# Performance work log

Hardware: AMD Instinct MI355X
Metric: run time of the kernel (lower is better)

The kernel has to match this reference:

```python
import jax, jax.numpy as jnp
import numpy as np

B, NA, F, K, L = 96, 48, 128, 64, 6
CUT = 5.0


def _forward(pos, f_in, emb, msg_w1, msg_b1, msg_w2, msg_b2, rbf_w, rbf_b,
             upd_U, upd_V, upd_w1, upd_b1, upd_w2, upd_b2,
             out_w1, out_b1, out_w2, out_b2, node_atom):
    p = pos.reshape(B, NA, 3)
    rij = p[:, :, None, :] - p[:, None, :, :]          # [B,n,n,3], pos_i - pos_j
    d2 = jnp.sum(rij * rij, -1)
    eye = jnp.eye(NA, dtype=bool)
    d = jnp.sqrt(jnp.where(eye, 1.0, d2))              # safe sqrt on diagonal
    mask = (~eye) & (d < CUT)                          # radius_graph, loop=False
    centers = jnp.linspace(0.0, CUT, K)
    gamma = 1.0 / ((CUT / K) ** 2 + 1e-9)
    rbf = jnp.exp(-gamma * (d[..., None] - centers) ** 2)   # [B,n,n,K]
    cutf = 0.5 * (jnp.cos(jnp.pi * d / CUT) + 1.0)          # cosine cutoff
    w_env = jnp.where(mask, cutf, 0.0)[..., None]
    dirv = rij / d[..., None]                               # unit directions
    s = emb[node_atom].reshape(B, NA, F)
    v = jnp.zeros((B, NA, 3, F), s.dtype)
    for l in range(L):
        # message block
        phi = jax.nn.silu(s @ msg_w1[l] + msg_b1[l]) @ msg_w2[l] + msg_b2[l]  # [B,n,3F]
        Wf = (rbf @ rbf_w[l] + rbf_b[l]) * w_env                              # [B,n,n,3F]
        x = phi[:, None, :, :] * Wf                                           # phi of sender j
        ds, dvv, dvs = jnp.split(x, 3, axis=-1)
        s = s + ds.sum(2)
        v = v + jnp.einsum('bijf,bjcf->bicf', dvv, v) \
              + jnp.einsum('bijf,bijc->bicf', dvs, dirv)
        # update block
        Uv = jnp.einsum('bncf,fg->bncg', v, upd_U[l])
        Vv = jnp.einsum('bncf,fg->bncg', v, upd_V[l])
        Vn = jnp.sqrt(jnp.sum(Vv * Vv, 2) + 1e-8)                             # [B,n,F]
        a = jax.nn.silu(jnp.concatenate([s, Vn], -1) @ upd_w1[l] + upd_b1[l]) @ upd_w2[l] + upd_b2[l]
        avv, asv, ass = jnp.split(a, 3, -1)
        v = v + avv[:, :, None, :] * Uv
        s = s + asv * jnp.sum(Uv * Vv, 2) + ass
    out = jax.nn.silu(s @ out_w1 + out_b1) @ out_w2 + out_b2                  # [B,n,1]
    return out.sum(1)                                                         # per-graph sum


def setup_inputs() -> dict:
    key = jax.random.key(0)
    ks = jax.random.split(key, 16)
    N = B * NA
    pos = jax.random.normal(ks[0], (N, 3), jnp.float32) * 2.0
    f_in = jnp.zeros((N, 1), jnp.float32)
    node_atom = jax.random.randint(ks[1], (N,), 1, 84)
    batch = jnp.arange(N) // NA
    g = lambda k, shp, fan: jax.random.normal(k, shp, jnp.float32) / np.sqrt(fan)
    return dict(
        f_in=f_in, pos=pos, batch=batch, node_atom=node_atom,
        emb=g(ks[2], (100, F), 1.0),
        msg_w1=g(ks[3], (L, F, F), F), msg_b1=jnp.zeros((L, F), jnp.float32),
        msg_w2=g(ks[4], (L, F, 3 * F), F), msg_b2=jnp.zeros((L, 3 * F), jnp.float32),
        rbf_w=g(ks[5], (L, K, 3 * F), K), rbf_b=jnp.zeros((L, 3 * F), jnp.float32),
        upd_U=g(ks[6], (L, F, F), F), upd_V=g(ks[7], (L, F, F), F),
        upd_w1=g(ks[8], (L, 2 * F, F), 2 * F), upd_b1=jnp.zeros((L, F), jnp.float32),
        upd_w2=g(ks[9], (L, F, 3 * F), F), upd_b2=jnp.zeros((L, 3 * F), jnp.float32),
        out_w1=g(ks[10], (F, F), F), out_b1=jnp.zeros((F,), jnp.float32),
        out_w2=g(ks[11], (F, 1), F), out_b2=jnp.zeros((1,), jnp.float32),
    )


def reference(f_in, pos, batch, node_atom, emb, msg_w1, msg_b1, msg_w2, msg_b2,
              rbf_w, rbf_b, upd_U, upd_V, upd_w1, upd_b1, upd_w2, upd_b2,
              out_w1, out_b1, out_w2, out_b2):
    return _forward(pos, f_in, emb, msg_w1, msg_b1, msg_w2, msg_b2, rbf_w, rbf_b,
                    upd_U, upd_V, upd_w1, upd_b1, upd_w2, upd_b2,
                    out_w1, out_b1, out_w2, out_b2, node_atom)
```

## Files before the change

kernel.cpp:

```cpp
#include <hip/hip_runtime.h>
#include <math.h>

#define NB 96
#define NA 48
#define NF 128
#define NK 64
#define NL 6
#define NN (NB*NA)
#define F3 (3*NF)
#define CUTF 5.0f
#define GAMMA_F ((float)(1.0 / (0.006103515625 + 1e-9)))
#define PI_F 3.14159265358979323846f

typedef __attribute__((ext_vector_type(8))) short short8;
typedef __attribute__((ext_vector_type(4))) float floatx4;

__device__ __forceinline__ float silu_f(float x) { return x / (1.0f + expf(-x)); }

__device__ __forceinline__ short f2bf(float x) {
    unsigned u = __builtin_bit_cast(unsigned, x);
    unsigned r = (u + 0x7fffu + ((u >> 16) & 1u)) >> 16;
    return (short)r;
}
__device__ __forceinline__ float bf2f(short h) {
    unsigned u = ((unsigned)(unsigned short)h) << 16;
    return __builtin_bit_cast(float, u);
}
__device__ __forceinline__ floatx4 mfma1(short8 a, short8 b, floatx4 c) {
    return __builtin_amdgcn_mfma_f32_16x16x32_bf16(a, b, c, 0, 0, 0);
}
__device__ __forceinline__ floatx4 mfma3(short8 ah, short8 al, short8 bh, short8 bl, floatx4 c) {
    c = __builtin_amdgcn_mfma_f32_16x16x32_bf16(ah, bh, c, 0, 0, 0);
    c = __builtin_amdgcn_mfma_f32_16x16x32_bf16(al, bh, c, 0, 0, 0);
    c = __builtin_amdgcn_mfma_f32_16x16x32_bf16(ah, bl, c, 0, 0, 0);
    return c;
}

__global__ void prep_kernel(const float* __restrict__ msg_w1, const float* __restrict__ msg_w2,
                            const float* __restrict__ rbf_w, const float* __restrict__ upd_U,
                            const float* __restrict__ upd_V, const float* __restrict__ upd_w1,
                            const float* __restrict__ upd_w2,
                            short* w1T_h, short* w1T_l, short* w2T_h, short* w2T_l,
                            short* rbfT_h, short* rbfT_l, short* UT_h, short* UT_l,
                            short* VT_h, short* VT_l, short* u1T_h, short* u1T_l,
                            short* u2T_h, short* u2T_l) {
    int m = blockIdx.y;
    int l = blockIdx.x / 384;
    int n = blockIdx.x % 384;
    const float* src; short* dh; short* dl; int K, N;
    switch (m) {
      case 0: src = msg_w1; dh = w1T_h; dl = w1T_l; K = NF;   N = NF; break;
      case 1: src = msg_w2; dh = w2T_h; dl = w2T_l; K = NF;   N = F3; break;
      case 2: src = rbf_w;  dh = rbfT_h;dl = rbfT_l;K = NK;   N = F3; break;
      case 3: src = upd_U;  dh = UT_h;  dl = UT_l;  K = NF;   N = NF; break;
      case 4: src = upd_V;  dh = VT_h;  dl = VT_l;  K = NF;   N = NF; break;
      case 5: src = upd_w1; dh = u1T_h; dl = u1T_l; K = 2*NF; N = NF; break;
      default:src = upd_w2; dh = u2T_h; dl = u2T_l; K = NF;   N = F3; break;
    }
    if (n >= N) return;
    for (int k = threadIdx.x; k < K; k += 64) {
        float x = src[((size_t)l*K + k)*N + n];
        short h = f2bf(x);
        size_t off = (size_t)l*N*K
                   + (size_t)((((n>>4)*(K>>5) + (k>>5))*4 + ((k>>3)&3))*128 + (n&15)*8 + (k&7));
        dh[off] = h;
        dl[off] = f2bf(x - bf2f(h));
    }
}

__global__ void __launch_bounds__(256) geom_kernel(const float* __restrict__ pos,
                                                   float* __restrict__ dG,
                                                   float* __restrict__ weG,
                                                   float* __restrict__ dirG) {
    int e = blockIdx.x*256 + threadIdx.x;
    int i = e / NA, j = e % NA;
    int b = i / NA, il = i % NA;
    int jg = b*NA + j;
    float dx = pos[i*3+0] - pos[jg*3+0];
    float dy = pos[i*3+1] - pos[jg*3+1];
    float dz = pos[i*3+2] - pos[jg*3+2];
    float d2 = dx*dx + dy*dy + dz*dz;
    float dd = sqrtf((j == il) ? 1.0f : d2);
    bool valid = (j != il) && (dd < CUTF);
    float we = valid ? 0.5f*(cosf(PI_F * dd / CUTF) + 1.0f) : 0.0f;
    dG[e] = dd;
    weG[e] = we;
    float inv = 1.0f / dd;
    dirG[0*(size_t)NN*NA + e] = dx*inv;
    dirG[1*(size_t)NN*NA + e] = dy*inv;
    dirG[2*(size_t)NN*NA + e] = dz*inv;
}

__global__ void zero_kernel(float* __restrict__ p) {
    p[(size_t)blockIdx.x * blockDim.x + threadIdx.x] = 0.f;
}

__global__ void __launch_bounds__(128) init_phi_kernel(
        const float* __restrict__ emb, const int* __restrict__ node_atom,
        const short* __restrict__ w1T_h, const short* __restrict__ w1T_l,
        const float* __restrict__ b1,
        const short* __restrict__ w2T_h, const short* __restrict__ w2T_l,
        const float* __restrict__ b2,
        float* __restrict__ s, float* __restrict__ v, float* __restrict__ phiT) {
    __shared__ short sH[16*NF], sL[16*NF];
    __shared__ short hH[16*NF], hL[16*NF];
    int t = threadIdx.x;
    int w = t >> 6, lane = t & 63, quad = lane >> 4, col = lane & 15;
    int n0 = blockIdx.x * 16;
    for (int e = t; e < 16*NF; e += 128) {
        int n = e >> 7, f = e & 127;
        int a = node_atom[n0+n];
        float x = emb[(size_t)a*NF + f];
        s[(size_t)(n0+n)*NF + f] = x;
        short h = f2bf(x);
        int ad = n*NF + (((f >> 3) ^ (n & 7)) << 3) + (f & 7);
        sH[ad] = h; sL[ad] = f2bf(x - bf2f(h));
    }
    for (int e = t; e < 16*F3; e += 128) v[(size_t)n0*F3 + e] = 0.f;
    __syncthreads();
    #pragma unroll
    for (int nt = 0; nt < 4; ++nt) {
        int fh = w*64 + nt*16 + col;
        floatx4 acc = (floatx4){0.f,0.f,0.f,0.f};
        #pragma unroll
        for (int ks = 0; ks < 4; ++ks) {
            int ad = col*NF + (((ks*4 + quad) ^ (col & 7)) << 3);
            size_t off = (size_t)((((w*4 + nt)*4 + ks)*4 + quad)*128) + col*8;
            acc = mfma3(*(short8*)&sH[ad], *(short8*)&sL[ad],
                        *(const short8*)(w1T_h + off), *(const short8*)(w1T_l + off), acc);
        }
        float bias = b1[fh];
        #pragma unroll
        for (int r = 0; r < 4; ++r) {
            int n = quad*4 + r;
            float hv = silu_f(acc[r] + bias);
            short h = f2bf(hv);
            int ad = n*NF + (((fh >> 3) ^ (n & 7)) << 3) + (fh & 7);
            hH[ad] = h; hL[ad] = f2bf(hv - bf2f(h));
        }
    }
    __syncthreads();
    #pragma unroll
    for (int nt = 0; nt < 12; ++nt) {
        int tt = w*192 + nt*16 + col;
        floatx4 acc = (floatx4){0.f,0.f,0.f,0.f};
        #pragma unroll
        for (int ks = 0; ks < 4; ++ks) {
            int ad = col*NF + (((ks*4 + quad) ^ (col & 7)) << 3);
            size_t off = (size_t)((((w*12 + nt)*4 + ks)*4 + quad)*128) + col*8;
            acc = mfma3(*(short8*)&hH[ad], *(short8*)&hL[ad],
                        *(const short8*)(w2T_h + off), *(const short8*)(w2T_l + off), acc);
        }
        float bias = b2[tt];
        floatx4 o;
        #pragma unroll
        for (int r = 0; r < 4; ++r) o[r] = acc[r] + bias;
        *(floatx4*)(phiT + (size_t)tt*NN + n0 + quad*4) = o;
    }
}

__global__ void __launch_bounds__(512) message_kernel(
        const float* __restrict__ sIn, const float* __restrict__ vIn,
        const float* __restrict__ phiT, const float* __restrict__ vT,
        const float* __restrict__ dG, const float* __restrict__ weG,
        const float* __restrict__ dirG,
        const short* __restrict__ rbfT_h,
        const float* __restrict__ rbf_b_l,
        float* __restrict__ sOut, float* __restrict__ vOut) {
    __shared__ short tkL[48*512];
    __shared__ float weL[8][NA];
    __shared__ float dirL[3][8][NA];
    int raw = blockIdx.x;
    int xcd = raw & 7, idx = raw >> 3;
    int graph = xcd + 8*(idx % 12);
    int itile = idx / 12;
    int i0l = itile*8, jbase = graph*NA;
    int n0 = jbase + i0l;
    int t = threadIdx.x;
    int w = t >> 6, lane = t & 63, quad = lane >> 4, col = lane & 15;
    int f = w*16 + col;
    float rb0 = rbf_b_l[f], rb1 = rbf_b_l[NF+f], rb2 = rbf_b_l[2*NF+f];
    short8 B[3][2];
    #pragma unroll
    for (int g = 0; g < 3; ++g)
        #pragma unroll
        for (int ks = 0; ks < 2; ++ks)
            B[g][ks] = *(const short8*)(rbfT_h + (size_t)((((g*8 + w)*2 + ks)*4 + quad)*128) + col*8);
    floatx4 ph0[3], ph1[3], ph2[3], vj0[3], vj1[3], vj2[3];
    #pragma unroll
    for (int mt = 0; mt < 3; ++mt) {
        int jq = jbase + mt*16 + quad*4;
        ph0[mt] = *(const floatx4*)(phiT + (size_t)f*NN + jq);
        ph1[mt] = *(const floatx4*)(phiT + (size_t)(NF+f)*NN + jq);
        ph2[mt] = *(const floatx4*)(phiT + (size_t)(2*NF+f)*NN + jq);
        vj0[mt] = *(const floatx4*)(vT + (size_t)(0*NF+f)*NN + jq);
        vj1[mt] = *(const floatx4*)(vT + (size_t)(1*NF+f)*NN + jq);
        vj2[mt] = *(const floatx4*)(vT + (size_t)(2*NF+f)*NN + jq);
    }
    for (int u = t; u < 768; u += 512) {
        int p = u >> 1, half = u & 1;
        int ii = p / NA, j = p % NA;
        int i = n0 + ii;
        float dd = dG[(size_t)i*NA + j];
        float we = weG[(size_t)i*NA + j];
        if (half == 0) {
            weL[ii][j] = we;
            dirL[0][ii][j] = dirG[0*(size_t)NN*NA + (size_t)i*NA + j];
            dirL[1][ii][j] = dirG[1*(size_t)NN*NA + (size_t)i*NA + j];
            dirL[2][ii][j] = dirG[2*(size_t)NN*NA + (size_t)i*NA + j];
        }
        int mt = j >> 4, colj = j & 15;
        int base = ((ii*3 + mt)*2 + half) << 9;
        #pragma unroll
        for (int c = 0; c < 4; ++c) {
            short8 h8;
            #pragma unroll
            for (int kk = 0; kk < 8; ++kk) {
                int k = half*32 + c*8 + kk;
                float cen = CUTF * (float)k / 63.0f;
                float df = dd - cen;
                h8[kk] = f2bf(__expf(-GAMMA_F * df * df) * we);
            }
            *(short8*)&tkL[base + (c*16 + colj)*8] = h8;
        }
    }
    __syncthreads();
    for (int ia = 0; ia < 8; ++ia) {
        floatx4 C[3][3];
        #pragma unroll
        for (int g = 0; g < 3; ++g)
            #pragma unroll
            for (int mt = 0; mt < 3; ++mt) C[g][mt] = (floatx4){0.f,0.f,0.f,0.f};
        #pragma unroll
        for (int mt = 0; mt < 3; ++mt) {
            #pragma unroll
            for (int ks = 0; ks < 2; ++ks) {
                short8 a = *(short8*)&tkL[(((ia*3 + mt)*2 + ks) << 9) + lane*8];
                #pragma unroll
                for (int g = 0; g < 3; ++g)
                    C[g][mt] = mfma1(a, B[g][ks], C[g][mt]);
            }
        }
        int i = n0 + ia;
        float accS = 0.f, av0 = 0.f, av1 = 0.f, av2 = 0.f;
        #pragma unroll
        for (int mt = 0; mt < 3; ++mt) {
            int jq = mt*16 + quad*4;
            floatx4 we4 = *(const floatx4*)&weL[ia][jq];
            floatx4 d0 = *(const floatx4*)&dirL[0][ia][jq];
            floatx4 d1 = *(const floatx4*)&dirL[1][ia][jq];
            floatx4 d2 = *(const floatx4*)&dirL[2][ia][jq];
            #pragma unroll
            for (int r = 0; r < 4; ++r) {
                float Wf0 = fmaf(rb0, we4[r], C[0][mt][r]);
                accS = fmaf(ph0[mt][r], Wf0, accS);
                float Wf1 = fmaf(rb1, we4[r], C[1][mt][r]);
                float x1 = ph1[mt][r] * Wf1;
                av0 = fmaf(x1, vj0[mt][r], av0);
                av1 = fmaf(x1, vj1[mt][r], av1);
                av2 = fmaf(x1, vj2[mt][r], av2);
                float Wf2 = fmaf(rb2, we4[r], C[2][mt][r]);
                float x2 = ph2[mt][r] * Wf2;
                av0 = fmaf(x2, d0[r], av0);
                av1 = fmaf(x2, d1[r], av1);
                av2 = fmaf(x2, d2[r], av2);
            }
        }
        accS += __shfl_xor(accS, 16, 64); accS += __shfl_xor(accS, 32, 64);
        av0 += __shfl_xor(av0, 16, 64);   av0 += __shfl_xor(av0, 32, 64);
        av1 += __shfl_xor(av1, 16, 64);   av1 += __shfl_xor(av1, 32, 64);
        av2 += __shfl_xor(av2, 16, 64);   av2 += __shfl_xor(av2, 32, 64);
        if (quad == 0) {
            sOut[(size_t)i*NF + f]        = sIn[(size_t)i*NF + f]        + accS;
            vOut[(size_t)i*F3 + f]        = vIn[(size_t)i*F3 + f]        + av0;
            vOut[(size_t)i*F3 + NF + f]   = vIn[(size_t)i*F3 + NF + f]   + av1;
            vOut[(size_t)i*F3 + 2*NF + f] = vIn[(size_t)i*F3 + 2*NF + f] + av2;
        }
    }
}

__global__ void __launch_bounds__(512) update_phi_kernel(
        const short* __restrict__ UT_h, const short* __restrict__ VT_h,
        const short* __restrict__ u1T_h, const float* __restrict__ b1,
        const short* __restrict__ u2T_h, const float* __restrict__ b2,
        float* __restrict__ s, float* __restrict__ v, float* __restrict__ vT,
        int doPhi,
        const short* __restrict__ pw1_h, const float* __restrict__ pb1,
        const short* __restrict__ pw2_h, const float* __restrict__ pb2,
        float* __restrict__ phiT) {
    __shared__ short A1h[48*NF], A1l[48*NF];
    __shared__ short A2h[16*256];
    __shared__ short hH[16*NF];
    __shared__ float sF[8*132];
    int t = threadIdx.x;
    int w = t >> 6, lane = t & 63, quad = lane >> 4, col = lane & 15;
    int raw = blockIdx.x;
    int xcd = raw & 7, idx = raw >> 3;
    int graph = xcd + 8*(idx % 12);
    int n0 = graph*NA + (idx / 12)*8;
    int f = w*16 + col;
    for (int e = t; e < 8*F3; e += 512) {
        int n = e / F3, cf = e % F3;
        int c = cf >> 7, ff = cf & 127;
        float x = v[(size_t)(n0+n)*F3 + cf];
        int row = c*16 + n;
        short h = f2bf(x);
        int ad = row*NF + (((ff >> 3) ^ (row & 7)) << 3) + (ff & 7);
        A1h[ad] = h; A1l[ad] = f2bf(x - bf2f(h));
    }
    for (int e = t; e < 8*NF; e += 512) {
        int n = e >> 7, ff = e & 127;
        float x = s[(size_t)(n0+n)*NF + ff];
        sF[n*132 + ff] = x;
        int ad = n*256 + (((ff >> 3) ^ (n & 7)) << 3) + (ff & 7);
        A2h[ad] = f2bf(x);
    }
    __syncthreads();
    floatx4 Uacc[3], Vacc[3];
    #pragma unroll
    for (int mt = 0; mt < 3; ++mt) { Uacc[mt] = (floatx4){0.f,0.f,0.f,0.f}; Vacc[mt] = (floatx4){0.f,0.f,0.f,0.f}; }
    #pragma unroll
    for (int ks = 0; ks < 4; ++ks) {
        size_t off = (size_t)(((w*4 + ks)*4 + quad)*128) + col*8;
        short8 BU = *(const short8*)(UT_h + off);
        short8 BV = *(const short8*)(VT_h + off);
        #pragma unroll
        for (int mt = 0; mt < 3; ++mt) {
            int row = mt*16 + col;
            int ad = row*NF + (((ks*4 + quad) ^ (row & 7)) << 3);
            short8 ah = *(short8*)&A1h[ad];
            Uacc[mt] = mfma1(ah, BU, Uacc[mt]);
            Vacc[mt] = mfma1(ah, BV, Vacc[mt]);
        }
    }
    if (quad < 2) {
        #pragma unroll
        for (int r = 0; r < 4; ++r) {
            int n = quad*4 + r;
            float v0 = Vacc[0][r], v1 = Vacc[1][r], v2 = Vacc[2][r];
            float vn = sqrtf(v0*v0 + v1*v1 + v2*v2 + 1e-8f);
            int ad = n*256 + ((((128 + f) >> 3) ^ (n & 7)) << 3) + (f & 7);
            A2h[ad] = f2bf(vn);
        }
    }
    __syncthreads();
    {
        floatx4 H = (floatx4){0.f,0.f,0.f,0.f};
        #pragma unroll
        for (int ks = 0; ks < 8; ++ks) {
            int ad = col*256 + (((ks*4 + quad) ^ (col & 7)) << 3);
            short8 ah = *(short8*)&A2h[ad];
            size_t off = (size_t)(((w*8 + ks)*4 + quad)*128) + col*8;
            H = mfma1(ah, *(const short8*)(u1T_h + off), H);
        }
        float bias = b1[f];
        if (quad < 2) {
            #pragma unroll
            for (int r = 0; r < 4; ++r) {
                int n = quad*4 + r;
                float hv = silu_f(H[r] + bias);
                int ad = n*NF + (((f >> 3) ^ (n & 7)) << 3) + (f & 7);
                hH[ad] = f2bf(hv);
            }
        }
    }
    __syncthreads();
    floatx4 O[3];
    #pragma unroll
    for (int gg = 0; gg < 3; ++gg) O[gg] = (floatx4){0.f,0.f,0.f,0.f};
    #pragma unroll
    for (int ks = 0; ks < 4; ++ks) {
        int ad = col*NF + (((ks*4 + quad) ^ (col & 7)) << 3);
        short8 ah = *(short8*)&hH[ad];
        #pragma unroll
        for (int gg = 0; gg < 3; ++gg) {
            size_t off = (size_t)((((gg*8 + w)*4 + ks)*4 + quad)*128) + col*8;
            O[gg] = mfma1(ah, *(const short8*)(u2T_h + off), O[gg]);
        }
    }
    __syncthreads();
    short* pH = A2h;
    if (quad < 2) {
        float bavv = b2[f], basv = b2[NF + f], bass = b2[2*NF + f];
        #pragma unroll
        for (int r = 0; r < 4; ++r) {
            int n = quad*4 + r;
            float avv = O[0][r] + bavv;
            float asv = O[1][r] + basv;
            float ass = O[2][r] + bass;
            float dot = Uacc[0][r]*Vacc[0][r] + Uacc[1][r]*Vacc[1][r] + Uacc[2][r]*Vacc[2][r];
            float snew = sF[n*132 + f] + asv*dot + ass;
            s[(size_t)(n0+n)*NF + f] = snew;
            int adS = n*NF + (((f >> 3) ^ (n & 7)) << 3) + (f & 7);
            pH[adS] = f2bf(snew);
            #pragma unroll
            for (int c = 0; c < 3; ++c) {
                int row = c*16 + n;
                int ad = row*NF + (((f >> 3) ^ (row & 7)) << 3) + (f & 7);
                float vold = bf2f(A1h[ad]) + bf2f(A1l[ad]);
                float vnew = vold + avv*Uacc[c][r];
                v[(size_t)(n0+n)*F3 + c*NF + f] = vnew;
                vT[(size_t)(c*NF + f)*NN + n0 + n] = vnew;
            }
        }
    }
    if (!doPhi) return;
    __syncthreads();
    {
        floatx4 acc = (floatx4){0.f,0.f,0.f,0.f};
        #pragma unroll
        for (int ks = 0; ks < 4; ++ks) {
            int ad = col*NF + (((ks*4 + quad) ^ (col & 7)) << 3);
            size_t off = (size_t)(((w*4 + ks)*4 + quad)*128) + col*8;
            acc = mfma1(*(short8*)&pH[ad], *(const short8*)(pw1_h + off), acc);
        }
        float bias = pb1[f];
        if (quad < 2) {
            #pragma unroll
            for (int r = 0; r < 4; ++r) {
                int n = quad*4 + r;
                float hv = silu_f(acc[r] + bias);
                int ad = n*NF + (((f >> 3) ^ (n & 7)) << 3) + (f & 7);
                hH[ad] = f2bf(hv);
            }
        }
    }
    __syncthreads();
    #pragma unroll
    for (int nt = 0; nt < 3; ++nt) {
        int tt = (w*3 + nt)*16 + col;
        floatx4 acc = (floatx4){0.f,0.f,0.f,0.f};
        #pragma unroll
        for (int ks = 0; ks < 4; ++ks) {
            int ad = col*NF + (((ks*4 + quad) ^ (col & 7)) << 3);
            size_t off = (size_t)((((w*3 + nt)*4 + ks)*4 + quad)*128) + col*8;
            acc = mfma1(*(short8*)&hH[ad], *(const short8*)(pw2_h + off), acc);
        }
        float bias = pb2[tt];
        if (quad < 2) {
            floatx4 o;
            #pragma unroll
            for (int r = 0; r < 4; ++r) o[r] = acc[r] + bias;
            *(floatx4*)(phiT + (size_t)tt*NN + n0 + quad*4) = o;
        }
    }
}

__global__ void zero_out_kernel(float* __restrict__ out) {
    out[threadIdx.x] = 0.f;
}

__global__ void out_kernel(const float* __restrict__ s,
                           const float* __restrict__ w1, const float* __restrict__ b1,
                           const float* __restrict__ w2, const float* __restrict__ b2,
                           float* __restrict__ out) {
    int n = blockIdx.x;
    int f = threadIdx.x;
    __shared__ float sh[NF];
    __shared__ float r2[2];
    sh[f] = s[n*NF + f];
    __syncthreads();
    float acc = b1[f];
    for (int g = 0; g < NF; ++g) acc = fmaf(sh[g], w1[g*NF + f], acc);
    float p = silu_f(acc) * w2[f];
    #pragma unroll
    for (int off = 32; off > 0; off >>= 1) p += __shfl_down(p, off, 64);
    if ((f & 63) == 0) r2[f >> 6] = p;
    __syncthreads();
    if (f == 0) atomicAdd(&out[n / NA], r2[0] + r2[1] + b2[0]);
}

extern "C" void kernel_launch(void* const* d_in, const int* in_sizes, int n_in,
                              void* d_out, int out_size, void* d_ws, size_t ws_size,
                              hipStream_t stream) {
    (void)in_sizes; (void)n_in; (void)out_size; (void)ws_size;
    const float* pos      = (const float*)d_in[1];
    const int*   node_atom= (const int*)  d_in[3];
    const float* emb      = (const float*)d_in[4];
    const float* msg_w1   = (const float*)d_in[5];
    const float* msg_b1   = (const float*)d_in[6];
    const float* msg_w2   = (const float*)d_in[7];
    const float* msg_b2   = (const float*)d_in[8];
    const float* rbf_w    = (const float*)d_in[9];
    const float* rbf_b    = (const float*)d_in[10];
    const float* upd_U    = (const float*)d_in[11];
    const float* upd_V    = (const float*)d_in[12];
    const float* upd_w1   = (const float*)d_in[13];
    const float* upd_b1   = (const float*)d_in[14];
    const float* upd_w2   = (const float*)d_in[15];
    const float* upd_b2   = (const float*)d_in[16];
    const float* out_w1   = (const float*)d_in[17];
    const float* out_b1   = (const float*)d_in[18];
    const float* out_w2   = (const float*)d_in[19];
    const float* out_b2   = (const float*)d_in[20];
    float* out = (float*)d_out;

    float* ws   = (float*)d_ws;
    float* sA   = ws; ws += (size_t)NN*NF;
    float* sB   = ws; ws += (size_t)NN*NF;
    float* vA   = ws; ws += (size_t)NN*F3;
    float* vB   = ws; ws += (size_t)NN*F3;
    float* phiT = ws; ws += (size_t)F3*NN;
    float* vT   = ws; ws += (size_t)F3*NN;
    float* dG   = ws; ws += (size_t)NN*NA;
    float* weG  = ws; ws += (size_t)NN*NA;
    float* dirG = ws; ws += (size_t)3*NN*NA;
    short* sp    = (short*)ws;
    short* w1T_h = sp; sp += (size_t)NL*NF*NF;
    short* w1T_l = sp; sp += (size_t)NL*NF*NF;
    short* w2T_h = sp; sp += (size_t)NL*F3*NF;
    short* w2T_l = sp; sp += (size_t)NL*F3*NF;
    short* rbfT_h= sp; sp += (size_t)NL*F3*NK;
    short* rbfT_l= sp; sp += (size_t)NL*F3*NK;
    short* UT_h  = sp; sp += (size_t)NL*NF*NF;
    short* UT_l  = sp; sp += (size_t)NL*NF*NF;
    short* VT_h  = sp; sp += (size_t)NL*NF*NF;
    short* VT_l  = sp; sp += (size_t)NL*NF*NF;
    short* u1T_h = sp; sp += (size_t)NL*NF*2*NF;
    short* u1T_l = sp; sp += (size_t)NL*NF*2*NF;
    short* u2T_h = sp; sp += (size_t)NL*F3*NF;
    short* u2T_l = sp; sp += (size_t)NL*F3*NF;

    prep_kernel<<<dim3(NL*384, 7), 64, 0, stream>>>(msg_w1, msg_w2, rbf_w, upd_U, upd_V, upd_w1, upd_w2,
                                                    w1T_h, w1T_l, w2T_h, w2T_l, rbfT_h, rbfT_l,
                                                    UT_h, UT_l, VT_h, VT_l, u1T_h, u1T_l, u2T_h, u2T_l);
    geom_kernel<<<(NN*NA)/256, 256, 0, stream>>>(pos, dG, weG, dirG);
    zero_kernel<<<(F3*NN)/256, 256, 0, stream>>>(vT);
    init_phi_kernel<<<NN/16, 128, 0, stream>>>(emb, node_atom,
                                               w1T_h, w1T_l, msg_b1, w2T_h, w2T_l, msg_b2,
                                               sA, vA, phiT);

    float* sC = sA; float* vC = vA; float* sN = sB; float* vN = vB;
    for (int l = 0; l < NL; ++l) {
        message_kernel<<<NB*6, 512, 0, stream>>>(sC, vC, phiT, vT,
                                                 dG, weG, dirG,
                                                 rbfT_h + (size_t)l*F3*NK,
                                                 rbf_b + (size_t)l*F3, sN, vN);
        int lp = (l + 1 < NL) ? (l + 1) : 0;
        update_phi_kernel<<<NN/8, 512, 0, stream>>>(
            UT_h + (size_t)l*NF*NF, VT_h + (size_t)l*NF*NF,
            u1T_h + (size_t)l*NF*2*NF, upd_b1 + (size_t)l*NF,
            u2T_h + (size_t)l*F3*NF, upd_b2 + (size_t)l*F3,
            sN, vN, vT,
            (l + 1 < NL) ? 1 : 0,
            w1T_h + (size_t)lp*NF*NF, msg_b1 + (size_t)lp*NF,
            w2T_h + (size_t)lp*F3*NF, msg_b2 + (size_t)lp*F3,
            phiT);
        float* tp;
        tp = sC; sC = sN; sN = tp;
        tp = vC; vC = vN; vN = tp;
    }
    zero_out_kernel<<<1, NB, 0, stream>>>(out);
    out_kernel<<<NN, NF, 0, stream>>>(sC, out_w1, out_b1, out_w2, out_b2, out);
}
```

Measured before the change: 596.3 us.

## Fuse all layers into one persistent per-graph kernel

```diff
diff --git a/kernel.cpp b/kernel.cpp
--- a/kernel.cpp
+++ b/kernel.cpp
@@ -159,289 +159,297 @@
     }
 }
 
-__global__ void __launch_bounds__(512) message_kernel(
-        const float* __restrict__ sIn, const float* __restrict__ vIn,
-        const float* __restrict__ phiT, const float* __restrict__ vT,
+__global__ void __launch_bounds__(512, 1) graph_kernel(
         const float* __restrict__ dG, const float* __restrict__ weG,
         const float* __restrict__ dirG,
-        const short* __restrict__ rbfT_h,
-        const float* __restrict__ rbf_b_l,
-        float* __restrict__ sOut, float* __restrict__ vOut) {
+        const short* __restrict__ rbfT_h_all, const float* __restrict__ rbf_b_all,
+        const short* __restrict__ UT_h_all, const short* __restrict__ VT_h_all,
+        const short* __restrict__ u1T_h_all, const float* __restrict__ ub1_all,
+        const short* __restrict__ u2T_h_all, const float* __restrict__ ub2_all,
+        const short* __restrict__ w1T_h_all, const float* __restrict__ pb1_all,
+        const short* __restrict__ w2T_h_all, const float* __restrict__ pb2_all,
+        float* sA, float* vA, float* sB, float* vB,
+        float* phiT, float* vT) {
     __shared__ short tkL[48*512];
     __shared__ float weL[8][NA];
     __shared__ float dirL[3][8][NA];
-    int raw = blockIdx.x;
-    int xcd = raw & 7, idx = raw >> 3;
-    int graph = xcd + 8*(idx % 12);
-    int itile = idx / 12;
-    int i0l = itile*8, jbase = graph*NA;
-    int n0 = jbase + i0l;
-    int t = threadIdx.x;
-    int w = t >> 6, lane = t & 63, quad = lane >> 4, col = lane & 15;
-    int f = w*16 + col;
-    float rb0 = rbf_b_l[f], rb1 = rbf_b_l[NF+f], rb2 = rbf_b_l[2*NF+f];
-    short8 B[3][2];
-    #pragma unroll
-    for (int g = 0; g < 3; ++g)
-        #pragma unroll
-        for (int ks = 0; ks < 2; ++ks)
-            B[g][ks] = *(const short8*)(rbfT_h + (size_t)((((g*8 + w)*2 + ks)*4 + quad)*128) + col*8);
-    floatx4 ph0[3], ph1[3], ph2[3], vj0[3], vj1[3], vj2[3];
-    #pragma unroll
-    for (int mt = 0; mt < 3; ++mt) {
-        int jq = jbase + mt*16 + quad*4;
-        ph0[mt] = *(const floatx4*)(phiT + (size_t)f*NN + jq);
-        ph1[mt] = *(const floatx4*)(phiT + (size_t)(NF+f)*NN + jq);
-        ph2[mt] = *(const floatx4*)(phiT + (size_t)(2*NF+f)*NN + jq);
-        vj0[mt] = *(const floatx4*)(vT + (size_t)(0*NF+f)*NN + jq);
-        vj1[mt] = *(const floatx4*)(vT + (size_t)(1*NF+f)*NN + jq);
-        vj2[mt] = *(const floatx4*)(vT + (size_t)(2*NF+f)*NN + jq);
-    }
-    for (int u = t; u < 768; u += 512) {
-        int p = u >> 1, half = u & 1;
-        int ii = p / NA, j = p % NA;
-        int i = n0 + ii;
-        float dd = dG[(size_t)i*NA + j];
-        float we = weG[(size_t)i*NA + j];
-        if (half == 0) {
-            weL[ii][j] = we;
-            dirL[0][ii][j] = dirG[0*(size_t)NN*NA + (size_t)i*NA + j];
-            dirL[1][ii][j] = dirG[1*(size_t)NN*NA + (size_t)i*NA + j];
-            dirL[2][ii][j] = dirG[2*(size_t)NN*NA + (size_t)i*NA + j];
-        }
-        int mt = j >> 4, colj = j & 15;
-        int base = ((ii*3 + mt)*2 + half) << 9;
-        #pragma unroll
-        for (int c = 0; c < 4; ++c) {
-            short8 h8;
-            #pragma unroll
-            for (int kk = 0; kk < 8; ++kk) {
-                int k = half*32 + c*8 + kk;
-                float cen = CUTF * (float)k / 63.0f;
-                float df = dd - cen;
-                h8[kk] = f2bf(__expf(-GAMMA_F * df * df) * we);
-            }
-            *(short8*)&tkL[base + (c*16 + colj)*8] = h8;
-        }
-    }
-    __syncthreads();
-    for (int ia = 0; ia < 8; ++ia) {
-        floatx4 C[3][3];
-        #pragma unroll
-        for (int g = 0; g < 3; ++g)
-            #pragma unroll
-            for (int mt = 0; mt < 3; ++mt) C[g][mt] = (floatx4){0.f,0.f,0.f,0.f};
-        #pragma unroll
-        for (int mt = 0; mt < 3; ++mt) {
-            #pragma unroll
-            for (int ks = 0; ks < 2; ++ks) {
-                short8 a = *(short8*)&tkL[(((ia*3 + mt)*2 + ks) << 9) + lane*8];
-                #pragma unroll
-                for (int g = 0; g < 3; ++g)
-                    C[g][mt] = mfma1(a, B[g][ks], C[g][mt]);
-            }
-        }
-        int i = n0 + ia;
-        float accS = 0.f, av0 = 0.f, av1 = 0.f, av2 = 0.f;
-        #pragma unroll
-        for (int mt = 0; mt < 3; ++mt) {
-            int jq = mt*16 + quad*4;
-            floatx4 we4 = *(const floatx4*)&weL[ia][jq];
-            floatx4 d0 = *(const floatx4*)&dirL[0][ia][jq];
-            floatx4 d1 = *(const floatx4*)&dirL[1][ia][jq];
-            floatx4 d2 = *(const floatx4*)&dirL[2][ia][jq];
-            #pragma unroll
-            for (int r = 0; r < 4; ++r) {
-                float Wf0 = fmaf(rb0, we4[r], C[0][mt][r]);
-                accS = fmaf(ph0[mt][r], Wf0, accS);
-                float Wf1 = fmaf(rb1, we4[r], C[1][mt][r]);
-                float x1 = ph1[mt][r] * Wf1;
-                av0 = fmaf(x1, vj0[mt][r], av0);
-                av1 = fmaf(x1, vj1[mt][r], av1);
-                av2 = fmaf(x1, vj2[mt][r], av2);
-                float Wf2 = fmaf(rb2, we4[r], C[2][mt][r]);
-                float x2 = ph2[mt][r] * Wf2;
-                av0 = fmaf(x2, d0[r], av0);
-                av1 = fmaf(x2, d1[r], av1);
-                av2 = fmaf(x2, d2[r], av2);
-            }
-        }
-        accS += __shfl_xor(accS, 16, 64); accS += __shfl_xor(accS, 32, 64);
-        av0 += __shfl_xor(av0, 16, 64);   av0 += __shfl_xor(av0, 32, 64);
-        av1 += __shfl_xor(av1, 16, 64);   av1 += __shfl_xor(av1, 32, 64);
-        av2 += __shfl_xor(av2, 16, 64);   av2 += __shfl_xor(av2, 32, 64);
-        if (quad == 0) {
-            sOut[(size_t)i*NF + f]        = sIn[(size_t)i*NF + f]        + accS;
-            vOut[(size_t)i*F3 + f]        = vIn[(size_t)i*F3 + f]        + av0;
-            vOut[(size_t)i*F3 + NF + f]   = vIn[(size_t)i*F3 + NF + f]   + av1;
-            vOut[(size_t)i*F3 + 2*NF + f] = vIn[(size_t)i*F3 + 2*NF + f] + av2;
-        }
-    }
-}
-
-__global__ void __launch_bounds__(512) update_phi_kernel(
-        const short* __restrict__ UT_h, const short* __restrict__ VT_h,
-        const short* __restrict__ u1T_h, const float* __restrict__ b1,
-        const short* __restrict__ u2T_h, const float* __restrict__ b2,
-        float* __restrict__ s, float* __restrict__ v, float* __restrict__ vT,
-        int doPhi,
-        const short* __restrict__ pw1_h, const float* __restrict__ pb1,
-        const short* __restrict__ pw2_h, const float* __restrict__ pb2,
-        float* __restrict__ phiT) {
     __shared__ short A1h[48*NF], A1l[48*NF];
     __shared__ short A2h[16*256];
     __shared__ short hH[16*NF];
     __shared__ float sF[8*132];
+    int graph = blockIdx.x;
+    int jbase = graph*NA;
     int t = threadIdx.x;
     int w = t >> 6, lane = t & 63, quad = lane >> 4, col = lane & 15;
-    int raw = blockIdx.x;
-    int xcd = raw & 7, idx = raw >> 3;
-    int graph = xcd + 8*(idx % 12);
-    int n0 = graph*NA + (idx / 12)*8;
     int f = w*16 + col;
-    for (int e = t; e < 8*F3; e += 512) {
-        int n = e / F3, cf = e % F3;
-        int c = cf >> 7, ff = cf & 127;
-        float x = v[(size_t)(n0+n)*F3 + cf];
-        int row = c*16 + n;
-        short h = f2bf(x);
-        int ad = row*NF + (((ff >> 3) ^ (row & 7)) << 3) + (ff & 7);
-        A1h[ad] = h; A1l[ad] = f2bf(x - bf2f(h));
-    }
-    for (int e = t; e < 8*NF; e += 512) {
-        int n = e >> 7, ff = e & 127;
-        float x = s[(size_t)(n0+n)*NF + ff];
-        sF[n*132 + ff] = x;
-        int ad = n*256 + (((ff >> 3) ^ (n & 7)) << 3) + (ff & 7);
-        A2h[ad] = f2bf(x);
-    }
-    __syncthreads();
-    floatx4 Uacc[3], Vacc[3];
-    #pragma unroll
-    for (int mt = 0; mt < 3; ++mt) { Uacc[mt] = (floatx4){0.f,0.f,0.f,0.f}; Vacc[mt] = (floatx4){0.f,0.f,0.f,0.f}; }
-    #pragma unroll
-    for (int ks = 0; ks < 4; ++ks) {
-        size_t off = (size_t)(((w*4 + ks)*4 + quad)*128) + col*8;
-        short8 BU = *(const short8*)(UT_h + off);
-        short8 BV = *(const short8*)(VT_h + off);
+
+    for (int l = 0; l < NL; ++l) {
+        const short* rbfT_h = rbfT_h_all + (size_t)l*F3*NK;
+        const float* rbf_b_l = rbf_b_all + (size_t)l*F3;
+        __syncthreads();
+        float rb0 = rbf_b_l[f], rb1 = rbf_b_l[NF+f], rb2 = rbf_b_l[2*NF+f];
+        short8 B[3][2];
+        #pragma unroll
+        for (int g = 0; g < 3; ++g)
+            #pragma unroll
+            for (int ks = 0; ks < 2; ++ks)
+                B[g][ks] = *(const short8*)(rbfT_h + (size_t)((((g*8 + w)*2 + ks)*4 + quad)*128) + col*8);
+        floatx4 ph0[3], ph1[3], ph2[3], vj0[3], vj1[3], vj2[3];
         #pragma unroll
         for (int mt = 0; mt < 3; ++mt) {
-            int row = mt*16 + col;
-            int ad = row*NF + (((ks*4 + quad) ^ (row & 7)) << 3);
-            short8 ah = *(short8*)&A1h[ad];
-            Uacc[mt] = mfma1(ah, BU, Uacc[mt]);
-            Vacc[mt] = mfma1(ah, BV, Vacc[mt]);
+            int jq = jbase + mt*16 + quad*4;
+            ph0[mt] = *(const floatx4*)(phiT + (size_t)f*NN + jq);
+            ph1[mt] = *(const floatx4*)(phiT + (size_t)(NF+f)*NN + jq);
+            ph2[mt] = *(const floatx4*)(phiT + (size_t)(2*NF+f)*NN + jq);
+            vj0[mt] = *(const floatx4*)(vT + (size_t)(0*NF+f)*NN + jq);
+            vj1[mt] = *(const floatx4*)(vT + (size_t)(1*NF+f)*NN + jq);
+            vj2[mt] = *(const floatx4*)(vT + (size_t)(2*NF+f)*NN + jq);
         }
-    }
-    if (quad < 2) {
-        #pragma unroll
-        for (int r = 0; r < 4; ++r) {
-            int n = quad*4 + r;
-            float v0 = Vacc[0][r], v1 = Vacc[1][r], v2 = Vacc[2][r];
-            float vn = sqrtf(v0*v0 + v1*v1 + v2*v2 + 1e-8f);
-            int ad = n*256 + ((((128 + f) >> 3) ^ (n & 7)) << 3) + (f & 7);
-            A2h[ad] = f2bf(vn);
+        for (int tile = 0; tile < 6; ++tile) {
+            int n0 = jbase + tile*8;
+            __syncthreads();
+            for (int u = t; u < 768; u += 512) {
+                int p = u >> 1, half = u & 1;
+                int ii = p / NA, j = p % NA;
+                int i = n0 + ii;
+                float dd = dG[(size_t)i*NA + j];
+                float we = weG[(size_t)i*NA + j];
+                if (half == 0) {
+                    weL[ii][j] = we;
+                    dirL[0][ii][j] = dirG[0*(size_t)NN*NA + (size_t)i*NA + j];
+                    dirL[1][ii][j] = dirG[1*(size_t)NN*NA + (size_t)i*NA + j];
+                    dirL[2][ii][j] = dirG[2*(size_t)NN*NA + (size_t)i*NA + j];
+                }
+                int mt = j >> 4, colj = j & 15;
+                int base = ((ii*3 + mt)*2 + half) << 9;
+                #pragma unroll
+                for (int c = 0; c < 4; ++c) {
+                    short8 h8;
+                    #pragma unroll
+                    for (int kk = 0; kk < 8; ++kk) {
+                        int k = half*32 + c*8 + kk;
+                        float cen = CUTF * (float)k / 63.0f;
+                        float df = dd - cen;
+                        h8[kk] = f2bf(__expf(-GAMMA_F * df * df) * we);
+                    }
+                    *(short8*)&tkL[base + (c*16 + colj)*8] = h8;
+                }
+            }
+            __syncthreads();
+            for (int ia = 0; ia < 8; ++ia) {
+                floatx4 C[3][3];
+                #pragma unroll
+                for (int g = 0; g < 3; ++g)
+                    #pragma unroll
+                    for (int mt = 0; mt < 3; ++mt) C[g][mt] = (floatx4){0.f,0.f,0.f,0.f};
+                #pragma unroll
+                for (int mt = 0; mt < 3; ++mt) {
+                    #pragma unroll
+                    for (int ks = 0; ks < 2; ++ks) {
+                        short8 a = *(short8*)&tkL[(((ia*3 + mt)*2 + ks) << 9) + lane*8];
+                        #pragma unroll
+                        for (int g = 0; g < 3; ++g)
+                            C[g][mt] = mfma1(a, B[g][ks], C[g][mt]);
+                    }
+                }
+                int i = n0 + ia;
+                float accS = 0.f, av0 = 0.f, av1 = 0.f, av2 = 0.f;
+                #pragma unroll
+                for (int mt = 0; mt < 3; ++mt) {
+                    int jq = mt*16 + quad*4;
+                    floatx4 we4 = *(const floatx4*)&weL[ia][jq];
+                    floatx4 d0 = *(const floatx4*)&dirL[0][ia][jq];
+                    floatx4 d1 = *(const floatx4*)&dirL[1][ia][jq];
+                    floatx4 d2 = *(const floatx4*)&dirL[2][ia][jq];
+                    #pragma unroll
+                    for (int r = 0; r < 4; ++r) {
+                        float Wf0 = fmaf(rb0, we4[r], C[0][mt][r]);
+                        accS = fmaf(ph0[mt][r], Wf0, accS);
+                        float Wf1 = fmaf(rb1, we4[r], C[1][mt][r]);
+                        float x1 = ph1[mt][r] * Wf1;
+                        av0 = fmaf(x1, vj0[mt][r], av0);
+                        av1 = fmaf(x1, vj1[mt][r], av1);
+                        av2 = fmaf(x1, vj2[mt][r], av2);
+                        float Wf2 = fmaf(rb2, we4[r], C[2][mt][r]);
+                        float x2 = ph2[mt][r] * Wf2;
+                        av0 = fmaf(x2, d0[r], av0);
+                        av1 = fmaf(x2, d1[r], av1);
+                        av2 = fmaf(x2, d2[r], av2);
+                    }
+                }
+                accS += __shfl_xor(accS, 16, 64); accS += __shfl_xor(accS, 32, 64);
+                av0 += __shfl_xor(av0, 16, 64);   av0 += __shfl_xor(av0, 32, 64);
+                av1 += __shfl_xor(av1, 16, 64);   av1 += __shfl_xor(av1, 32, 64);
+                av2 += __shfl_xor(av2, 16, 64);   av2 += __shfl_xor(av2, 32, 64);
+                if (quad == 0) {
+                    sB[(size_t)i*NF + f]        = sA[(size_t)i*NF + f]        + accS;
+                    vB[(size_t)i*F3 + f]        = vA[(size_t)i*F3 + f]        + av0;
+                    vB[(size_t)i*F3 + NF + f]   = vA[(size_t)i*F3 + NF + f]   + av1;
+                    vB[(size_t)i*F3 + 2*NF + f] = vA[(size_t)i*F3 + 2*NF + f] + av2;
+                }
+            }
         }
-    }
-    __syncthreads();
-    {
-        floatx4 H = (floatx4){0.f,0.f,0.f,0.f};
-        #pragma unroll
-        for (int ks = 0; ks < 8; ++ks) {
-            int ad = col*256 + (((ks*4 + quad) ^ (col & 7)) << 3);
-            short8 ah = *(short8*)&A2h[ad];
-            size_t off = (size_t)(((w*8 + ks)*4 + quad)*128) + col*8;
-            H = mfma1(ah, *(const short8*)(u1T_h + off), H);
-        }
-        float bias = b1[f];
-        if (quad < 2) {
+        int doPhi = (l + 1 < NL);
+        int lp = doPhi ? (l + 1) : 0;
+        const short* UT_h  = UT_h_all  + (size_t)l*NF*NF;
+        const short* VT_h  = VT_h_all  + (size_t)l*NF*NF;
+        const short* u1T_h = u1T_h_all + (size_t)l*NF*2*NF;
+        const float* b1u   = ub1_all   + (size_t)l*NF;
+        const short* u2T_h = u2T_h_all + (size_t)l*F3*NF;
+        const float* b2u   = ub2_all   + (size_t)l*F3;
+        const short* pw1_h = w1T_h_all + (size_t)lp*NF*NF;
+        const float* pb1   = pb1_all   + (size_t)lp*NF;
+        const short* pw2_h = w2T_h_all + (size_t)lp*F3*NF;
+        const float* pb2   = pb2_all   + (size_t)lp*F3;
+        for (int tile = 0; tile < 6; ++tile) {
+            int n0 = jbase + tile*8;
+            __syncthreads();
+            for (int e = t; e < 8*F3; e += 512) {
+                int n = e / F3, cf = e % F3;
+                int c = cf >> 7, ff = cf & 127;
+                float x = vB[(size_t)(n0+n)*F3 + cf];
+                int row = c*16 + n;
+                short h = f2bf(x);
+                int ad = row*NF + (((ff >> 3) ^ (row & 7)) << 3) + (ff & 7);
+                A1h[ad] = h; A1l[ad] = f2bf(x - bf2f(h));
+            }
+            for (int e = t; e < 8*NF; e += 512) {
+                int n = e >> 7, ff = e & 127;
+                float x = sB[(size_t)(n0+n)*NF + ff];
+                sF[n*132 + ff] = x;
+                int ad = n*256 + (((ff >> 3) ^ (n & 7)) << 3) + (ff & 7);
+                A2h[ad] = f2bf(x);
+            }
+            __syncthreads();
+            floatx4 Uacc[3], Vacc[3];
             #pragma unroll
-            for (int r = 0; r < 4; ++r) {
-                int n = quad*4 + r;
-                float hv = silu_f(H[r] + bias);
-                int ad = n*NF + (((f >> 3) ^ (n & 7)) << 3) + (f & 7);
-                hH[ad] = f2bf(hv);
-            }
-        }
-    }
-    __syncthreads();
-    floatx4 O[3];
-    #pragma unroll
-    for (int gg = 0; gg < 3; ++gg) O[gg] = (floatx4){0.f,0.f,0.f,0.f};
-    #pragma unroll
-    for (int ks = 0; ks < 4; ++ks) {
-        int ad = col*NF + (((ks*4 + quad) ^ (col & 7)) << 3);
-        short8 ah = *(short8*)&hH[ad];
-        #pragma unroll
-        for (int gg = 0; gg < 3; ++gg) {
-            size_t off = (size_t)((((gg*8 + w)*4 + ks)*4 + quad)*128) + col*8;
-            O[gg] = mfma1(ah, *(const short8*)(u2T_h + off), O[gg]);
-        }
-    }
-    __syncthreads();
-    short* pH = A2h;
-    if (quad < 2) {
-        float bavv = b2[f], basv = b2[NF + f], bass = b2[2*NF + f];
-        #pragma unroll
-        for (int r = 0; r < 4; ++r) {
-            int n = quad*4 + r;
-            float avv = O[0][r] + bavv;
-            float asv = O[1][r] + basv;
-            float ass = O[2][r] + bass;
-            float dot = Uacc[0][r]*Vacc[0][r] + Uacc[1][r]*Vacc[1][r] + Uacc[2][r]*Vacc[2][r];
-            float snew = sF[n*132 + f] + asv*dot + ass;
-            s[(size_t)(n0+n)*NF + f] = snew;
-            int adS = n*NF + (((f >> 3) ^ (n & 7)) << 3) + (f & 7);
-            pH[adS] = f2bf(snew);
+            for (int mt = 0; mt < 3; ++mt) { Uacc[mt] = (floatx4){0.f,0.f,0.f,0.f}; Vacc[mt] = (floatx4){0.f,0.f,0.f,0.f}; }
             #pragma unroll
-            for (int c = 0; c < 3; ++c) {
-                int row = c*16 + n;
-                int ad = row*NF + (((f >> 3) ^ (row & 7)) << 3) + (f & 7);
-                float vold = bf2f(A1h[ad]) + bf2f(A1l[ad]);
-                float vnew = vold + avv*Uacc[c][r];
-                v[(size_t)(n0+n)*F3 + c*NF + f] = vnew;
-                vT[(size_t)(c*NF + f)*NN + n0 + n] = vnew;
-            }
-        }
-    }
-    if (!doPhi) return;
-    __syncthreads();
-    {
-        floatx4 acc = (floatx4){0.f,0.f,0.f,0.f};
-        #pragma unroll
-        for (int ks = 0; ks < 4; ++ks) {
-            int ad = col*NF + (((ks*4 + quad) ^ (col & 7)) << 3);
-            size_t off = (size_t)(((w*4 + ks)*4 + quad)*128) + col*8;
-            acc = mfma1(*(short8*)&pH[ad], *(const short8*)(pw1_h + off), acc);
-        }
-        float bias = pb1[f];
-        if (quad < 2) {
+            for (int ks = 0; ks < 4; ++ks) {
+                size_t off = (size_t)(((w*4 + ks)*4 + quad)*128) + col*8;
+                short8 BU = *(const short8*)(UT_h + off);
+                short8 BV = *(const short8*)(VT_h + off);
+                #pragma unroll
+                for (int mt = 0; mt < 3; ++mt) {
+                    int row = mt*16 + col;
+                    int ad = row*NF + (((ks*4 + quad) ^ (row & 7)) << 3);
+                    short8 ah = *(short8*)&A1h[ad];
+                    Uacc[mt] = mfma1(ah, BU, Uacc[mt]);
+                    Vacc[mt] = mfma1(ah, BV, Vacc[mt]);
+                }
+            }
+            if (quad < 2) {
+                #pragma unroll
+                for (int r = 0; r < 4; ++r) {
+                    int n = quad*4 + r;
+                    float v0 = Vacc[0][r], v1 = Vacc[1][r], v2 = Vacc[2][r];
+                    float vn = sqrtf(v0*v0 + v1*v1 + v2*v2 + 1e-8f);
+                    int ad = n*256 + ((((128 + f) >> 3) ^ (n & 7)) << 3) + (f & 7);
+                    A2h[ad] = f2bf(vn);
+                }
+            }
+            __syncthreads();
+            {
+                floatx4 H = (floatx4){0.f,0.f,0.f,0.f};
+                #pragma unroll
+                for (int ks = 0; ks < 8; ++ks) {
+                    int ad = col*256 + (((ks*4 + quad) ^ (col & 7)) << 3);
+                    short8 ah = *(short8*)&A2h[ad];
+                    size_t off = (size_t)(((w*8 + ks)*4 + quad)*128) + col*8;
+                    H = mfma1(ah, *(const short8*)(u1T_h + off), H);
+                }
+                float bias = b1u[f];
+                if (quad < 2) {
+                    #pragma unroll
+                    for (int r = 0; r < 4; ++r) {
+                        int n = quad*4 + r;
+                        float hv = silu_f(H[r] + bias);
+                        int ad = n*NF + (((f >> 3) ^ (n & 7)) << 3) + (f & 7);
+                        hH[ad] = f2bf(hv);
+                    }
+                }
+            }
+            __syncthreads();
+            floatx4 O[3];
             #pragma unroll
-            for (int r = 0; r < 4; ++r) {
-                int n = quad*4 + r;
-                float hv = silu_f(acc[r] + bias);
-                int ad = n*NF + (((f >> 3) ^ (n & 7)) << 3) + (f & 7);
-                hH[ad] = f2bf(hv);
-            }
-        }
-    }
-    __syncthreads();
-    #pragma unroll
-    for (int nt = 0; nt < 3; ++nt) {
-        int tt = (w*3 + nt)*16 + col;
-        floatx4 acc = (floatx4){0.f,0.f,0.f,0.f};
-        #pragma unroll
-        for (int ks = 0; ks < 4; ++ks) {
-            int ad = col*NF + (((ks*4 + quad) ^ (col & 7)) << 3);
-            size_t off = (size_t)((((w*3 + nt)*4 + ks)*4 + quad)*128) + col*8;
-            acc = mfma1(*(short8*)&hH[ad], *(const short8*)(pw2_h + off), acc);
-        }
-        float bias = pb2[tt];
-        if (quad < 2) {
-            floatx4 o;
+            for (int gg = 0; gg < 3; ++gg) O[gg] = (floatx4){0.f,0.f,0.f,0.f};
             #pragma unroll
-            for (int r = 0; r < 4; ++r) o[r] = acc[r] + bias;
-            *(floatx4*)(phiT + (size_t)tt*NN + n0 + quad*4) = o;
+            for (int ks = 0; ks < 4; ++ks) {
+                int ad = col*NF + (((ks*4 + quad) ^ (col & 7)) << 3);
+                short8 ah = *(short8*)&hH[ad];
+                #pragma unroll
+                for (int gg = 0; gg < 3; ++gg) {
+                    size_t off = (size_t)((((gg*8 + w)*4 + ks)*4 + quad)*128) + col*8;
+                    O[gg] = mfma1(ah, *(const short8*)(u2T_h + off), O[gg]);
+                }
+            }
+            __syncthreads();
+            short* pH = A2h;
+            if (quad < 2) {
+                float bavv = b2u[f], basv = b2u[NF + f], bass = b2u[2*NF + f];
+                #pragma unroll
+                for (int r = 0; r < 4; ++r) {
+                    int n = quad*4 + r;
+                    float avv = O[0][r] + bavv;
+                    float asv = O[1][r] + basv;
+                    float ass = O[2][r] + bass;
+                    float dot = Uacc[0][r]*Vacc[0][r] + Uacc[1][r]*Vacc[1][r] + Uacc[2][r]*Vacc[2][r];
+                    float snew = sF[n*132 + f] + asv*dot + ass;
+                    sA[(size_t)(n0+n)*NF + f] = snew;
+                    int adS = n*NF + (((f >> 3) ^ (n & 7)) << 3) + (f & 7);
+                    pH[adS] = f2bf(snew);
+                    #pragma unroll
+                    for (int c = 0; c < 3; ++c) {
+                        int row = c*16 + n;
+                        int ad = row*NF + (((f >> 3) ^ (row & 7)) << 3) + (f & 7);
+                        float vold = bf2f(A1h[ad]) + bf2f(A1l[ad]);
+                        float vnew = vold + avv*Uacc[c][r];
+                        vA[(size_t)(n0+n)*F3 + c*NF + f] = vnew;
+                        vT[(size_t)(c*NF + f)*NN + n0 + n] = vnew;
+                    }
+                }
+            }
+            if (doPhi) {
+                __syncthreads();
+                {
+                    floatx4 acc = (floatx4){0.f,0.f,0.f,0.f};
+                    #pragma unroll
+                    for (int ks = 0; ks < 4; ++ks) {
+                        int ad = col*NF + (((ks*4 + quad) ^ (col & 7)) << 3);
+                        size_t off = (size_t)(((w*4 + ks)*4 + quad)*128) + col*8;
+                        acc = mfma1(*(short8*)&pH[ad], *(const short8*)(pw1_h + off), acc);
+                    }
+                    float bias = pb1[f];
+                    if (quad < 2) {
+                        #pragma unroll
+                        for (int r = 0; r < 4; ++r) {
+                            int n = quad*4 + r;
+                            float hv = silu_f(acc[r] + bias);
+                            int ad = n*NF + (((f >> 3) ^ (n & 7)) << 3) + (f & 7);
+                            hH[ad] = f2bf(hv);
+                        }
+                    }
+                }
+                __syncthreads();
+                #pragma unroll
+                for (int nt = 0; nt < 3; ++nt) {
+                    int tt = (w*3 + nt)*16 + col;
+                    floatx4 acc = (floatx4){0.f,0.f,0.f,0.f};
+                    #pragma unroll
+                    for (int ks = 0; ks < 4; ++ks) {
+                        int ad = col*NF + (((ks*4 + quad) ^ (col & 7)) << 3);
+                        size_t off = (size_t)((((w*3 + nt)*4 + ks)*4 + quad)*128) + col*8;
+                        acc = mfma1(*(short8*)&hH[ad], *(const short8*)(pw2_h + off), acc);
+                    }
+                    float bias = pb2[tt];
+                    if (quad < 2) {
+                        floatx4 o;
+                        #pragma unroll
+                        for (int r = 0; r < 4; ++r) o[r] = acc[r] + bias;
+                        *(floatx4*)(phiT + (size_t)tt*NN + n0 + quad*4) = o;
+                    }
+                }
+            }
         }
     }
 }
@@ -530,26 +538,12 @@
                                                w1T_h, w1T_l, msg_b1, w2T_h, w2T_l, msg_b2,
                                                sA, vA, phiT);
 
-    float* sC = sA; float* vC = vA; float* sN = sB; float* vN = vB;
-    for (int l = 0; l < NL; ++l) {
-        message_kernel<<<NB*6, 512, 0, stream>>>(sC, vC, phiT, vT,
-                                                 dG, weG, dirG,
-                                                 rbfT_h + (size_t)l*F3*NK,
-                                                 rbf_b + (size_t)l*F3, sN, vN);
-        int lp = (l + 1 < NL) ? (l + 1) : 0;
-        update_phi_kernel<<<NN/8, 512, 0, stream>>>(
-            UT_h + (size_t)l*NF*NF, VT_h + (size_t)l*NF*NF,
-            u1T_h + (size_t)l*NF*2*NF, upd_b1 + (size_t)l*NF,
-            u2T_h + (size_t)l*F3*NF, upd_b2 + (size_t)l*F3,
-            sN, vN, vT,
-            (l + 1 < NL) ? 1 : 0,
-            w1T_h + (size_t)lp*NF*NF, msg_b1 + (size_t)lp*NF,
-            w2T_h + (size_t)lp*F3*NF, msg_b2 + (size_t)lp*F3,
-            phiT);
-        float* tp;
-        tp = sC; sC = sN; sN = tp;
-        tp = vC; vC = vN; vN = tp;
-    }
+    graph_kernel<<<NB, 512, 0, stream>>>(dG, weG, dirG,
+                                         rbfT_h, rbf_b,
+                                         UT_h, VT_h, u1T_h, upd_b1, u2T_h, upd_b2,
+                                         w1T_h, msg_b1, w2T_h, msg_b2,
+                                         sA, vA, sB, vB, phiT, vT);
+
     zero_out_kernel<<<1, NB, 0, stream>>>(out);
-    out_kernel<<<NN, NF, 0, stream>>>(sC, out_w1, out_b1, out_w2, out_b2, out);
-}
+    out_kernel<<<NN, NF, 0, stream>>>(sA, out_w1, out_b1, out_w2, out_b2, out);
+}
```

New measurement: 1.167 ms. 1.96x slower.
